# Performance work log

Hardware: AMD Instinct MI355X
Metric: run time of the kernel (lower is better)

The kernel has to match this reference:

```python
import jax, jax.numpy as jnp
import numpy as np

BN_EPS = 1e-5
ATT_EPS = 1e-6


def _conv(x, w, groups=1):
    # x: [B,C,H,W], w: [O, C//groups, k, k], stride 1, SAME padding for odd k
    k = w.shape[-1]
    p = (k - 1) // 2
    return jax.lax.conv_general_dilated(
        x, w, window_strides=(1, 1), padding=[(p, p), (p, p)],
        dimension_numbers=('NCHW', 'OIHW', 'NCHW'), feature_group_count=groups)


def _bn(x, bnp):
    # bnp: [4, C] stacked (scale, bias, running_mean, running_var); eval-mode BN
    s, b, m, v = bnp[0], bnp[1], bnp[2], bnp[3]
    inv = s / jnp.sqrt(v + BN_EPS)
    return x * inv[None, :, None, None] + (b - m * inv)[None, :, None, None]


def _relu6(x):
    return jnp.clip(x, 0.0, 6.0)


def _ffn(x, fc1_w, fc1_bn, conv1_w, conv1_bn, conv2_w, conv2_bn, fc2_w, fc2_bn):
    # E_FFN: 1x1 ConvBNReLU6 -> dw5x5 ConvBNReLU6 & dw3x3 ConvBNReLU6 -> sum -> 1x1 ConvBN -> ReLU6
    C = x.shape[1]
    h = _relu6(_bn(_conv(x, fc1_w), fc1_bn))
    x1 = _relu6(_bn(_conv(h, conv1_w, groups=C), conv1_bn))
    x2 = _relu6(_bn(_conv(h, conv2_w, groups=C), conv2_bn))
    return _relu6(_bn(_conv(x1 + x2, fc2_w), fc2_bn))


def _bias(y, b):
    return y + b[None, :, None, None]


def setup_inputs() -> dict:
    key = jax.random.key(0)
    ks = jax.random.split(key, 16)
    C, M = 64, 8  # in_places, in_places // scale
    B, H, W = 4, 224, 224

    def w(k, shape, s=0.05):
        return (jax.random.normal(k, shape, dtype=jnp.float32) * s)

    def bn_params(k, c):
        k1, k2, k3, k4 = jax.random.split(k, 4)
        scale = 1.0 + 0.1 * jax.random.normal(k1, (c,), dtype=jnp.float32)
        bias = 0.1 * jax.random.normal(k2, (c,), dtype=jnp.float32)
        mean = 0.1 * jax.random.normal(k3, (c,), dtype=jnp.float32)
        var = 1.0 + 0.1 * jax.random.uniform(k4, (c,), dtype=jnp.float32)
        return jnp.stack([scale, bias, mean, var])  # [4, c]

    return {
        'x': jax.random.normal(ks[0], (B, C, H, W), dtype=jnp.float32),
        'gamma': jnp.full((1,), 0.5, dtype=jnp.float32),  # nonzero so attention branch matters
        'q_w': w(ks[1], (M, C, 1, 1)), 'q_b': w(ks[2], (M,)),
        'k_w': w(ks[3], (M, C, 1, 1)), 'k_b': w(ks[4], (M,)),
        'v_w': w(ks[5], (C, C, 1, 1)), 'v_b': w(ks[6], (C,)),
        'fc1_w': w(ks[7], (C, C, 1, 1)), 'fc1_bn': bn_params(ks[8], C),
        'conv1_w': w(ks[9], (C, 1, 5, 5)), 'conv1_bn': bn_params(ks[10], C),
        'conv2_w': w(ks[11], (C, 1, 3, 3)), 'conv2_bn': bn_params(ks[12], C),
        'fc2_w': w(ks[13], (C, C, 1, 1)), 'fc2_bn': bn_params(ks[14], C),
    }


def reference(x, gamma, q_w, q_b, k_w, k_b, v_w, v_b,
              fc1_w, fc1_bn, conv1_w, conv1_bn, conv2_w, conv2_bn, fc2_w, fc2_bn):
    B, C, H, W = x.shape
    N = H * W
    x_channel = _ffn(x, fc1_w, fc1_bn, conv1_w, conv1_bn, conv2_w, conv2_bn, fc2_w, fc2_bn)
    # softplus feature maps; Q,K: [B, m, N]
    Q = jax.nn.softplus(_bias(_conv(x, q_w), q_b).reshape(B, -1, N))
    K = jax.nn.softplus(_bias(_conv(x, k_w), k_b).reshape(B, -1, N))
    V = (_bias(_conv(x, v_w), v_b) + x_channel).reshape(B, C, N)
    Qt = jnp.swapaxes(Q, 1, 2)                              # [B, N, m]
    KV = jnp.einsum('bmn,bcn->bmc', K, V)                   # [B, m, C]
    norm = 1.0 / jnp.einsum('bnm,bm->bn', Qt, K.sum(-1) + ATT_EPS)  # [B, N]
    wv = jnp.einsum('bnm,bmc,bn->bcn', Qt, KV, norm).reshape(B, C, H, W)
    return x + gamma * wv
```

## Files before the change

### kernel.cpp

```cpp
#include <hip/hip_runtime.h>
#include <math.h>

#define B_ 4
#define C_ 64
#define M_ 8
#define H_ 224
#define W_ 224
#define N_ (H_*W_)
#define CN_ (C_*N_)
#define MN_ (M_*N_)
#define BCN_ (B_*CN_)
#define BMN_ (B_*MN_)

typedef __attribute__((ext_vector_type(8))) short short8;
typedef __attribute__((ext_vector_type(4))) float f32x4;
typedef __attribute__((ext_vector_type(4))) unsigned int uint4v;

__device__ __forceinline__ float relu6f(float v){ return fminf(fmaxf(v,0.0f),6.0f); }
__device__ __forceinline__ float softplusf(float v){
  return v > 0.0f ? v + log1pf(expf(-v)) : log1pf(expf(v));
}
__device__ __forceinline__ unsigned int rne2(float lo, float hi){
  unsigned int ul = __float_as_uint(lo); ul += 0x7FFFu + ((ul>>16)&1u);
  unsigned int uh = __float_as_uint(hi); uh += 0x7FFFu + ((uh>>16)&1u);
  return (ul>>16) | (uh & 0xFFFF0000u);
}

#define FMA4(A, W, X) { A.x = fmaf((W), (X).x, A.x); A.y = fmaf((W), (X).y, A.y); \
                        A.z = fmaf((W), (X).z, A.z); A.w = fmaf((W), (X).w, A.w); }

__global__ __launch_bounds__(256) void k_fc1k(const float* __restrict__ x,
                                              const float* __restrict__ w,
                                              const float* __restrict__ bn,
                                              const float* __restrict__ kw,
                                              const float* __restrict__ kb,
                                              float* __restrict__ h,
                                              float* __restrict__ Kq)
{
  __shared__ float xsl[2*1024];
  __shared__ float wl [2*512];
  __shared__ float kt [512];
  const int tid  = threadIdx.x;
  const int b    = blockIdx.x / 392;
  const int pg   = blockIdx.x % 392;
  const int pix0 = pg*128;
  const float* xb = x + (size_t)b*CN_ + pix0;

  for (int idx = tid; idx < 512; idx += 256) {
    const int c = idx >> 3, m = idx & 7;
    kt[idx] = kw[m*64 + c];
  }

  const int scp = tid >> 5;
  const int spx = (tid & 31) << 2;
  const int e0 = tid*2, e1 = tid*2+1;
  const int wc0 = e0 >> 6, wo0 = e0 & 63;
  const int wc1 = e1 >> 6, wo1 = e1 & 63;

  {
    const float4 xr = *(const float4*)(xb + (size_t)scp*N_ + spx);
    const float w0r = w[wo0*64 + wc0];
    const float w1r = w[wo1*64 + wc1];
    *(float4*)&xsl[scp*128 + spx] = xr;
    wl[e0] = w0r; wl[e1] = w1r;
  }
  __syncthreads();

  const int lane = tid & 63, wv_ = tid >> 6;
  const int och  = 2*wv_ + (lane >> 5);
  const int ocb  = och*8;
  const int px4  = (lane & 31) << 2;

  float4 ah[8];
  float4 ak = {0,0,0,0};
  #pragma unroll
  for (int i = 0; i < 8; ++i) ah[i] = make_float4(0.f,0.f,0.f,0.f);

  for (int ck = 0; ck < 8; ++ck) {
    const int cur = ck & 1, nxt = cur ^ 1;
    const float* xc = &xsl[cur*1024];
    const float* wc = &wl[cur*512];
    float4 xr; float w0r, w1r;
    if (ck < 7) {
      const int c0n = (ck+1)*8;
      xr  = *(const float4*)(xb + (size_t)(c0n + scp)*N_ + spx);
      w0r = w[wo0*64 + c0n + wc0];
      w1r = w[wo1*64 + c0n + wc1];
    }
    #pragma unroll
    for (int cp = 0; cp < 8; ++cp) {
      const float4 xv = *(const float4*)&xc[cp*128 + px4];
      const float4 w0 = *(const float4*)&wc[cp*64 + ocb];
      const float4 w1 = *(const float4*)&wc[cp*64 + ocb + 4];
      const float kvw = kt[(ck*8+cp)*8 + och];
      FMA4(ah[0], w0.x, xv); FMA4(ah[1], w0.y, xv);
      FMA4(ah[2], w0.z, xv); FMA4(ah[3], w0.w, xv);
      FMA4(ah[4], w1.x, xv); FMA4(ah[5], w1.y, xv);
      FMA4(ah[6], w1.z, xv); FMA4(ah[7], w1.w, xv);
      FMA4(ak, kvw, xv);
    }
    if (ck < 7) {
      *(float4*)&xsl[nxt*1024 + scp*128 + spx] = xr;
      wl[nxt*512 + e0] = w0r; wl[nxt*512 + e1] = w1r;
    }
    __syncthreads();
  }

  float* hb = h + (size_t)b*CN_ + pix0 + px4;
  #pragma unroll
  for (int o = 0; o < 8; ++o) {
    const int oc = ocb + o;
    const float inv  = bn[oc] / sqrtf(bn[192+oc] + 1e-5f);
    const float beta = bn[64+oc] - bn[128+oc]*inv;
    float4 o4;
    o4.x = relu6f(fmaf(ah[o].x, inv, beta));
    o4.y = relu6f(fmaf(ah[o].y, inv, beta));
    o4.z = relu6f(fmaf(ah[o].z, inv, beta));
    o4.w = relu6f(fmaf(ah[o].w, inv, beta));
    *(float4*)(hb + (size_t)oc*N_) = o4;
  }
  {
    const float kbm = kb[och];
    float4 q;
    q.x = softplusf(ak.x + kbm); q.y = softplusf(ak.y + kbm);
    q.z = softplusf(ak.z + kbm); q.w = softplusf(ak.w + kbm);
    *(float4*)(Kq + (size_t)b*MN_ + (size_t)och*N_ + pix0 + px4) = q;
  }
}

__global__ __launch_bounds__(256) void k_dw(const float* __restrict__ h,
                                            const float* __restrict__ w5,
                                            const float* __restrict__ w3,
                                            const float* __restrict__ bn1,
                                            const float* __restrict__ bn2,
                                            float* __restrict__ s)
{
  __shared__ float tile[36*37];
  const int tid = threadIdx.x;
  const int blk = blockIdx.x;
  const int t   = blk % 49;
  const int bc  = blk / 49;
  const int c   = bc & 63;
  const int tx0 = (t % 7) * 32;
  const int ty0 = (t / 7) * 32;
  const float* hb = h + (size_t)bc * N_;

  for (int idx = tid; idx < 1296; idx += 256) {
    const int ly = idx / 36, lx = idx - ly*36;
    const int gy = ty0 + ly - 2, gx = tx0 + lx - 2;
    float v = 0.0f;
    if (gy >= 0 && gy < H_ && gx >= 0 && gx < W_) v = hb[gy*W_ + gx];
    tile[ly*37 + lx] = v;
  }
  __syncthreads();

  float w5r[25], w3r[9];
  #pragma unroll
  for (int i = 0; i < 25; ++i) w5r[i] = w5[c*25 + i];
  #pragma unroll
  for (int i = 0; i < 9; ++i)  w3r[i] = w3[c*9 + i];
  const float inv1 = bn1[c] / sqrtf(bn1[192+c] + 1e-5f);
  const float bet1 = bn1[64+c] - bn1[128+c]*inv1;
  const float inv2 = bn2[c] / sqrtf(bn2[192+c] + 1e-5f);
  const float bet2 = bn2[64+c] - bn2[128+c]*inv2;

  const int ty  = tid >> 3;
  const int tx4 = (tid & 7) << 2;
  float a5[4] = {0,0,0,0}, a3[4] = {0,0,0,0};
  #pragma unroll
  for (int dy = 0; dy < 5; ++dy) {
    float r[8];
    #pragma unroll
    for (int i = 0; i < 8; ++i) r[i] = tile[(ty+dy)*37 + tx4 + i];
    #pragma unroll
    for (int dx = 0; dx < 5; ++dx) {
      const float wv = w5r[dy*5+dx];
      #pragma unroll
      for (int p = 0; p < 4; ++p) a5[p] = fmaf(wv, r[p+dx], a5[p]);
    }
    if (dy >= 1 && dy <= 3) {
      #pragma unroll
      for (int dx = 1; dx <= 3; ++dx) {
        const float wv = w3r[(dy-1)*3+(dx-1)];
        #pragma unroll
        for (int p = 0; p < 4; ++p) a3[p] = fmaf(wv, r[p+dx], a3[p]);
      }
    }
  }
  float* sb = s + (size_t)bc * N_ + (ty0+ty)*W_ + tx0 + tx4;
  float4 o4;
  o4.x = relu6f(fmaf(a5[0],inv1,bet1)) + relu6f(fmaf(a3[0],inv2,bet2));
  o4.y = relu6f(fmaf(a5[1],inv1,bet1)) + relu6f(fmaf(a3[1],inv2,bet2));
  o4.z = relu6f(fmaf(a5[2],inv1,bet1)) + relu6f(fmaf(a3[2],inv2,bet2));
  o4.w = relu6f(fmaf(a5[3],inv1,bet1)) + relu6f(fmaf(a3[3],inv2,bet2));
  *(float4*)sb = o4;
}

__device__ __forceinline__ short8 bfrag(const unsigned short* __restrict__ L,
                                        int px, int c0){
  const unsigned short* p = L + c0*128 + px;
  unsigned int w0 = (unsigned int)p[0]   | ((unsigned int)p[128]<<16);
  unsigned int w1 = (unsigned int)p[256] | ((unsigned int)p[384]<<16);
  unsigned int w2 = (unsigned int)p[512] | ((unsigned int)p[640]<<16);
  unsigned int w3 = (unsigned int)p[768] | ((unsigned int)p[896]<<16);
  uint4v q = {w0,w1,w2,w3};
  return __builtin_bit_cast(short8, q);
}
__device__ __forceinline__ short8 afrag(const float* __restrict__ W, int idx){
  const float4 f0 = *(const float4*)(W + idx);
  const float4 f1 = *(const float4*)(W + idx + 4);
  uint4v q = {rne2(f0.x,f0.y), rne2(f0.z,f0.w), rne2(f1.x,f1.y), rne2(f1.z,f1.w)};
  return __builtin_bit_cast(short8, q);
}

__global__ __launch_bounds__(256) void k_v(const float* __restrict__ x,
                                           const float* __restrict__ s,
                                           const float* __restrict__ vw,
                                           const float* __restrict__ vb,
                                           const float* __restrict__ fw,
                                           const float* __restrict__ fbn,
                                           float* __restrict__ V)
{
  __shared__ unsigned short xls[64*128];
  __shared__ unsigned short sls[64*128];
  __shared__ float invb[3][64];
  const int tid  = threadIdx.x;
  const int b    = blockIdx.x / 392;
  const int pg   = blockIdx.x % 392;
  const int pix0 = pg*128;
  const float* xb = x + (size_t)b*CN_ + pix0;
  const float* sb = s + (size_t)b*CN_ + pix0;

  const int scp = tid >> 5;
  const int spx = (tid & 31) << 2;
  #pragma unroll
  for (int i = 0; i < 8; ++i) {
    const int c = i*8 + scp;
    const float4 xr = *(const float4*)(xb + (size_t)c*N_ + spx);
    const float4 sr = *(const float4*)(sb + (size_t)c*N_ + spx);
    *(uint2*)&xls[c*128 + spx] = make_uint2(rne2(xr.x,xr.y), rne2(xr.z,xr.w));
    *(uint2*)&sls[c*128 + spx] = make_uint2(rne2(sr.x,sr.y), rne2(sr.z,sr.w));
  }
  if (tid < 64) {
    const float inv = fbn[tid] / sqrtf(fbn[192+tid] + 1e-5f);
    invb[0][tid] = inv;
    invb[1][tid] = fbn[64+tid] - fbn[128+tid]*inv;
    invb[2][tid] = vb[tid];
  }
  __syncthreads();

  const int lane = tid & 63, wv = tid >> 6;
  const int l15 = lane & 15, u = lane >> 4;
  const int pxw = wv*32;

  f32x4 av[4][2], af[4][2];
  #pragma unroll
  for (int t = 0; t < 4; ++t)
    #pragma unroll
    for (int s2 = 0; s2 < 2; ++s2) { av[t][s2] = (f32x4){0.f,0.f,0.f,0.f};
                                     af[t][s2] = (f32x4){0.f,0.f,0.f,0.f}; }

  #pragma unroll
  for (int kk = 0; kk < 2; ++kk) {
    const int c0 = kk*32 + u*8;
    {
      const short8 a0 = afrag(vw, (0*16+l15)*64 + c0);
      const short8 a1 = afrag(vw, (1*16+l15)*64 + c0);
      const short8 a2 = afrag(vw, (2*16+l15)*64 + c0);
      const short8 a3 = afrag(vw, (3*16+l15)*64 + c0);
      #pragma unroll
      for (int s2 = 0; s2 < 2; ++s2) {
        const short8 bx = bfrag(xls, pxw + s2*16 + l15, c0);
        av[0][s2] = __builtin_amdgcn_mfma_f32_16x16x32_bf16(a0, bx, av[0][s2], 0,0,0);
        av[1][s2] = __builtin_amdgcn_mfma_f32_16x16x32_bf16(a1, bx, av[1][s2], 0,0,0);
        av[2][s2] = __builtin_amdgcn_mfma_f32_16x16x32_bf16(a2, bx, av[2][s2], 0,0,0);
        av[3][s2] = __builtin_amdgcn_mfma_f32_16x16x32_bf16(a3, bx, av[3][s2], 0,0,0);
      }
    }
    {
      const short8 a0 = afrag(fw, (0*16+l15)*64 + c0);
      const short8 a1 = afrag(fw, (1*16+l15)*64 + c0);
      const short8 a2 = afrag(fw, (2*16+l15)*64 + c0);
      const short8 a3 = afrag(fw, (3*16+l15)*64 + c0);
      #pragma unroll
      for (int s2 = 0; s2 < 2; ++s2) {
        const short8 bs = bfrag(sls, pxw + s2*16 + l15, c0);
        af[0][s2] = __builtin_amdgcn_mfma_f32_16x16x32_bf16(a0, bs, af[0][s2], 0,0,0);
        af[1][s2] = __builtin_amdgcn_mfma_f32_16x16x32_bf16(a1, bs, af[1][s2], 0,0,0);
        af[2][s2] = __builtin_amdgcn_mfma_f32_16x16x32_bf16(a2, bs, af[2][s2], 0,0,0);
        af[3][s2] = __builtin_amdgcn_mfma_f32_16x16x32_bf16(a3, bs, af[3][s2], 0,0,0);
      }
    }
  }

  float* Vb = V + (size_t)b*CN_ + pix0;
  #pragma unroll
  for (int t = 0; t < 4; ++t) {
    #pragma unroll
    for (int s2 = 0; s2 < 2; ++s2) {
      const int px = pxw + s2*16 + l15;
      #pragma unroll
      for (int r = 0; r < 4; ++r) {
        const int oc = t*16 + u*4 + r;
        Vb[(size_t)oc*N_ + px] = av[t][s2][r] + invb[2][oc]
            + relu6f(fmaf(af[t][s2][r], invb[0][oc], invb[1][oc]));
      }
    }
  }
}

__global__ __launch_bounds__(256) void k_kv(const float* __restrict__ V,
                                            const float* __restrict__ Kq,
                                            float* __restrict__ KV,
                                            float* __restrict__ Ksum)
{
  const int blk = blockIdx.x;
  const int b   = blk >> 7;
  const int rem = blk & 127;
  const int cg  = rem >> 4;
  const int ch  = rem & 15;
  const int tid = threadIdx.x;
  const int base = ch * 3136;
  const int end  = base + 3136;
  const float* Kb = Kq + (size_t)b*MN_;
  const float* Vb = V  + (size_t)b*CN_ + (size_t)(cg*8)*N_;

  float acc[64];
  #pragma unroll
  for (int i = 0; i < 64; ++i) acc[i] = 0.0f;
  float ks[8] = {0,0,0,0,0,0,0,0};

  for (int n4 = base + tid*4; n4 < end; n4 += 1024) {
    float4 kr[8];
    #pragma unroll
    for (int m2 = 0; m2 < 8; ++m2) kr[m2] = *(const float4*)(Kb + (size_t)m2*N_ + n4);
    #pragma unroll
    for (int m2 = 0; m2 < 8; ++m2)
      ks[m2] += (kr[m2].x + kr[m2].y) + (kr[m2].z + kr[m2].w);
    #pragma unroll
    for (int c8 = 0; c8 < 8; ++c8) {
      const float4 vv = *(const float4*)(Vb + (size_t)c8*N_ + n4);
      #pragma unroll
      for (int m2 = 0; m2 < 8; ++m2) {
        float t = acc[m2*8+c8];
        t = fmaf(kr[m2].x, vv.x, t);
        t = fmaf(kr[m2].y, vv.y, t);
        t = fmaf(kr[m2].z, vv.z, t);
        t = fmaf(kr[m2].w, vv.w, t);
        acc[m2*8+c8] = t;
      }
    }
  }
  const int lane = tid & 63;

  {
    int nv = 64;
    #pragma unroll
    for (int mask = 1; mask <= 32; mask <<= 1) {
      nv >>= 1;
      const bool hi = (lane & mask) != 0;
      #pragma unroll
      for (int i = 0; i < 32; ++i) {
        if (i < nv) {
          const float mine = hi ? acc[i] : acc[i+nv];
          const float th = __shfl_xor(mine, mask);
          acc[i] = (hi ? acc[i+nv] : acc[i]) + th;
        }
      }
    }
  }
  const int j = 32*(lane & 1) + 16*((lane >> 1) & 1) + 8*((lane >> 2) & 1)
              + 4*((lane >> 3) & 1) + 2*((lane >> 4) & 1) + ((lane >> 5) & 1);
  atomicAdd(&KV[b*512 + (j >> 3)*64 + cg*8 + (j & 7)], acc[0]);

  if (cg == 0) {
    float mk = 0.0f;
    #pragma unroll
    for (int jj = 0; jj < 8; ++jj) {
      float v = ks[jj];
      v += __shfl_xor(v, 1);
      v += __shfl_xor(v, 2);
      v += __shfl_xor(v, 4);
      v += __shfl_xor(v, 8);
      v += __shfl_xor(v, 16);
      v += __shfl_xor(v, 32);
      if (lane == jj) mk = v;
    }
    if (lane < 8) atomicAdd(&Ksum[b*8 + lane], mk);
  }
}

__global__ __launch_bounds__(256) void k_out(const float* __restrict__ x,
                                             const float* __restrict__ qw,
                                             const float* __restrict__ qb,
                                             const float* __restrict__ gamma,
                                             const float* __restrict__ KV,
                                             const float* __restrict__ Ksum,
                                             float* __restrict__ out)
{
  __shared__ float xs[64*128];
  __shared__ __align__(16) float kvt[64*8];
  __shared__ __align__(16) float qwt[64*8];
  __shared__ float qs[8][128];
  __shared__ float scl[128];
  __shared__ float ksl[8];
  const int tid = threadIdx.x;
  const int b  = blockIdx.x / 392;
  const int pg = blockIdx.x % 392;
  const int pix0 = pg*128;
  const float* xb = x + (size_t)b*CN_ + pix0;

  for (int idx = tid; idx < 512; idx += 256) {
    const int m = idx >> 6, c = idx & 63;
    kvt[c*8 + m] = KV[b*512 + idx];
    qwt[c*8 + m] = qw[idx];
  }
  if (tid < 8) ksl[tid] = Ksum[b*8 + tid] + 1e-6f;
  #pragma unroll
  for (int i = 0; i < 8; ++i) {
    const int idx = i*256 + tid;
    const int c = idx >> 5, p4 = (idx & 31) << 2;
    const float4 v = *(const float4*)(xb + (size_t)c*N_ + p4);
    *(float4*)&xs[c*128 + p4] = v;
  }
  __syncthreads();

  if (tid < 128) {
    const int px = tid;
    float q[8] = {0,0,0,0,0,0,0,0};
    #pragma unroll 8
    for (int c = 0; c < 64; ++c) {
      const float xv = xs[c*128 + px];
      const float4 w0 = *(const float4*)&qwt[c*8];
      const float4 w1 = *(const float4*)&qwt[c*8+4];
      q[0] = fmaf(w0.x, xv, q[0]);
      q[1] = fmaf(w0.y, xv, q[1]);
      q[2] = fmaf(w0.z, xv, q[2]);
      q[3] = fmaf(w0.w, xv, q[3]);
      q[4] = fmaf(w1.x, xv, q[4]);
      q[5] = fmaf(w1.y, xv, q[5]);
      q[6] = fmaf(w1.z, xv, q[6]);
      q[7] = fmaf(w1.w, xv, q[7]);
    }
    float den = 0.0f;
    #pragma unroll
    for (int m = 0; m < 8; ++m) {
      q[m] = softplusf(q[m] + qb[m]);
      den  = fmaf(q[m], ksl[m], den);
      qs[m][px] = q[m];
    }
    scl[px] = gamma[0] / den;
  }
  __syncthreads();

  float* ob = out + (size_t)b*CN_ + pix0;
  #pragma unroll
  for (int i = 0; i < 32; ++i) {
    const int idx = i*256 + tid;
    const int c = idx >> 7, px = idx & 127;
    const float4 k0 = *(const float4*)&kvt[c*8];
    const float4 k1 = *(const float4*)&kvt[c*8+4];
    float wv;
    wv = qs[0][px]*k0.x;
    wv = fmaf(qs[1][px], k0.y, wv);
    wv = fmaf(qs[2][px], k0.z, wv);
    wv = fmaf(qs[3][px], k0.w, wv);
    wv = fmaf(qs[4][px], k1.x, wv);
    wv = fmaf(qs[5][px], k1.y, wv);
    wv = fmaf(qs[6][px], k1.z, wv);
    wv = fmaf(qs[7][px], k1.w, wv);
    ob[(size_t)c*N_ + px] = fmaf(scl[px], wv, xs[c*128 + px]);
  }
}

extern "C" void kernel_launch(void* const* d_in, const int* in_sizes, int n_in,
                              void* d_out, int out_size, void* d_ws, size_t ws_size,
                              hipStream_t stream) {
  const float* x      = (const float*)d_in[0];
  const float* gamma  = (const float*)d_in[1];
  const float* q_w    = (const float*)d_in[2];
  const float* q_b    = (const float*)d_in[3];
  const float* k_w    = (const float*)d_in[4];
  const float* k_b    = (const float*)d_in[5];
  const float* v_w    = (const float*)d_in[6];
  const float* v_b    = (const float*)d_in[7];
  const float* fc1_w  = (const float*)d_in[8];
  const float* fc1_bn = (const float*)d_in[9];
  const float* c1_w   = (const float*)d_in[10];
  const float* c1_bn  = (const float*)d_in[11];
  const float* c2_w   = (const float*)d_in[12];
  const float* c2_bn  = (const float*)d_in[13];
  const float* fc2_w  = (const float*)d_in[14];
  const float* fc2_bn = (const float*)d_in[15];
  float* outp = (float*)d_out;

  float* ws   = (float*)d_ws;
  float* bufA = ws;
  float* bufS = ws + (size_t)BCN_;
  float* bufK = ws + (size_t)2*BCN_;
  float* kv   = ws + (size_t)2*BCN_ + BMN_;
  float* ksum = kv + 2048;

  hipMemsetAsync(kv, 0, (2048 + 32)*sizeof(float), stream);

  k_fc1k<<<dim3(B_*392), dim3(256), 0, stream>>>(x, fc1_w, fc1_bn, k_w, k_b, bufA, bufK);
  k_dw  <<<dim3(B_*C_*49), dim3(256), 0, stream>>>(bufA, c1_w, c2_w, c1_bn, c2_bn, bufS);
  k_v   <<<dim3(B_*392), dim3(256), 0, stream>>>(x, bufS, v_w, v_b, fc2_w, fc2_bn, bufA);
  k_kv  <<<dim3(512), dim3(256), 0, stream>>>(bufA, bufK, kv, ksum);
  k_out <<<dim3(B_*392), dim3(256), 0, stream>>>(x, q_w, q_b, gamma, kv, ksum, outp);
}
```

Measured before the change: 302.4 us.

## Compute fc1 and K projections with bf16 MFMA instead of fp32 FMAs

The fused fc1+K 1x1 conv kernel is rewritten to stage x as bf16 in shared memory and run the 64x64 fc1 and 8x64 K projections on 16x16x32 bf16 MFMA instructions, with the K rows padded into a fifth A tile. This replaces the fp32 FMA loop and its double-buffered x/weight staging. BN scale and shift are precomputed per block into shared memory. Output stores become scalar per-pixel writes rather than float4, and bf16 rounding of x and the weights reduces precision.

```diff
diff --git a/kernel.cpp b/kernel.cpp
--- a/kernel.cpp
+++ b/kernel.cpp
@@ -26,8 +26,26 @@
   return (ul>>16) | (uh & 0xFFFF0000u);
 }
 
-#define FMA4(A, W, X) { A.x = fmaf((W), (X).x, A.x); A.y = fmaf((W), (X).y, A.y); \
-                        A.z = fmaf((W), (X).z, A.z); A.w = fmaf((W), (X).w, A.w); }
+__device__ __forceinline__ short8 bfrag(const unsigned short* __restrict__ L,
+                                        int px, int c0){
+  const unsigned short* p = L + c0*128 + px;
+  unsigned int w0 = (unsigned int)p[0]   | ((unsigned int)p[128]<<16);
+  unsigned int w1 = (unsigned int)p[256] | ((unsigned int)p[384]<<16);
+  unsigned int w2 = (unsigned int)p[512] | ((unsigned int)p[640]<<16);
+  unsigned int w3 = (unsigned int)p[768] | ((unsigned int)p[896]<<16);
+  uint4v q = {w0,w1,w2,w3};
+  return __builtin_bit_cast(short8, q);
+}
+__device__ __forceinline__ short8 afrag(const float* __restrict__ W, int idx){
+  const float4 f0 = *(const float4*)(W + idx);
+  const float4 f1 = *(const float4*)(W + idx + 4);
+  uint4v q = {rne2(f0.x,f0.y), rne2(f0.z,f0.w), rne2(f1.x,f1.y), rne2(f1.z,f1.w)};
+  return __builtin_bit_cast(short8, q);
+}
+__device__ __forceinline__ short8 zfrag(){
+  uint4v q = {0u,0u,0u,0u};
+  return __builtin_bit_cast(short8, q);
+}
 
 __global__ __launch_bounds__(256) void k_fc1k(const float* __restrict__ x,
                                               const float* __restrict__ w,
@@ -37,94 +55,82 @@
                                               float* __restrict__ h,
                                               float* __restrict__ Kq)
 {
-  __shared__ float xsl[2*1024];
-  __shared__ float wl [2*512];
-  __shared__ float kt [512];
+  __shared__ unsigned short xls[64*128];
+  __shared__ float invb[2][64];
   const int tid  = threadIdx.x;
   const int b    = blockIdx.x / 392;
   const int pg   = blockIdx.x % 392;
   const int pix0 = pg*128;
   const float* xb = x + (size_t)b*CN_ + pix0;
 
-  for (int idx = tid; idx < 512; idx += 256) {
-    const int c = idx >> 3, m = idx & 7;
-    kt[idx] = kw[m*64 + c];
-  }
-
   const int scp = tid >> 5;
   const int spx = (tid & 31) << 2;
-  const int e0 = tid*2, e1 = tid*2+1;
-  const int wc0 = e0 >> 6, wo0 = e0 & 63;
-  const int wc1 = e1 >> 6, wo1 = e1 & 63;
-
-  {
-    const float4 xr = *(const float4*)(xb + (size_t)scp*N_ + spx);
-    const float w0r = w[wo0*64 + wc0];
-    const float w1r = w[wo1*64 + wc1];
-    *(float4*)&xsl[scp*128 + spx] = xr;
-    wl[e0] = w0r; wl[e1] = w1r;
+  #pragma unroll
+  for (int i = 0; i < 8; ++i) {
+    const int c = i*8 + scp;
+    const float4 xr = *(const float4*)(xb + (size_t)c*N_ + spx);
+    *(uint2*)&xls[c*128 + spx] = make_uint2(rne2(xr.x,xr.y), rne2(xr.z,xr.w));
+  }
+  if (tid < 64) {
+    const float inv = bn[tid] / sqrtf(bn[192+tid] + 1e-5f);
+    invb[0][tid] = inv;
+    invb[1][tid] = bn[64+tid] - bn[128+tid]*inv;
   }
   __syncthreads();
 
-  const int lane = tid & 63, wv_ = tid >> 6;
-  const int och  = 2*wv_ + (lane >> 5);
-  const int ocb  = och*8;
-  const int px4  = (lane & 31) << 2;
-
-  float4 ah[8];
-  float4 ak = {0,0,0,0};
-  #pragma unroll
-  for (int i = 0; i < 8; ++i) ah[i] = make_float4(0.f,0.f,0.f,0.f);
-
-  for (int ck = 0; ck < 8; ++ck) {
-    const int cur = ck & 1, nxt = cur ^ 1;
-    const float* xc = &xsl[cur*1024];
-    const float* wc = &wl[cur*512];
-    float4 xr; float w0r, w1r;
-    if (ck < 7) {
-      const int c0n = (ck+1)*8;
-      xr  = *(const float4*)(xb + (size_t)(c0n + scp)*N_ + spx);
-      w0r = w[wo0*64 + c0n + wc0];
-      w1r = w[wo1*64 + c0n + wc1];
-    }
-    #pragma unroll
-    for (int cp = 0; cp < 8; ++cp) {
-      const float4 xv = *(const float4*)&xc[cp*128 + px4];
-      const float4 w0 = *(const float4*)&wc[cp*64 + ocb];
-      const float4 w1 = *(const float4*)&wc[cp*64 + ocb + 4];
-      const float kvw = kt[(ck*8+cp)*8 + och];
-      FMA4(ah[0], w0.x, xv); FMA4(ah[1], w0.y, xv);
-      FMA4(ah[2], w0.z, xv); FMA4(ah[3], w0.w, xv);
-      FMA4(ah[4], w1.x, xv); FMA4(ah[5], w1.y, xv);
-      FMA4(ah[6], w1.z, xv); FMA4(ah[7], w1.w, xv);
-      FMA4(ak, kvw, xv);
-    }
-    if (ck < 7) {
-      *(float4*)&xsl[nxt*1024 + scp*128 + spx] = xr;
-      wl[nxt*512 + e0] = w0r; wl[nxt*512 + e1] = w1r;
-    }
-    __syncthreads();
-  }
-
-  float* hb = h + (size_t)b*CN_ + pix0 + px4;
-  #pragma unroll
-  for (int o = 0; o < 8; ++o) {
-    const int oc = ocb + o;
-    const float inv  = bn[oc] / sqrtf(bn[192+oc] + 1e-5f);
-    const float beta = bn[64+oc] - bn[128+oc]*inv;
-    float4 o4;
-    o4.x = relu6f(fmaf(ah[o].x, inv, beta));
-    o4.y = relu6f(fmaf(ah[o].y, inv, beta));
-    o4.z = relu6f(fmaf(ah[o].z, inv, beta));
-    o4.w = relu6f(fmaf(ah[o].w, inv, beta));
-    *(float4*)(hb + (size_t)oc*N_) = o4;
-  }
-  {
-    const float kbm = kb[och];
-    float4 q;
-    q.x = softplusf(ak.x + kbm); q.y = softplusf(ak.y + kbm);
-    q.z = softplusf(ak.z + kbm); q.w = softplusf(ak.w + kbm);
-    *(float4*)(Kq + (size_t)b*MN_ + (size_t)och*N_ + pix0 + px4) = q;
+  const int lane = tid & 63, wv = tid >> 6;
+  const int l15 = lane & 15, u = lane >> 4;
+  const int pxw = wv*32;
+
+  f32x4 acc[5][2];
+  #pragma unroll
+  for (int t = 0; t < 5; ++t)
+    #pragma unroll
+    for (int s2 = 0; s2 < 2; ++s2) acc[t][s2] = (f32x4){0.f,0.f,0.f,0.f};
+
+  #pragma unroll
+  for (int kk = 0; kk < 2; ++kk) {
+    const int c0 = kk*32 + u*8;
+    const short8 a0 = afrag(w, (0*16+l15)*64 + c0);
+    const short8 a1 = afrag(w, (1*16+l15)*64 + c0);
+    const short8 a2 = afrag(w, (2*16+l15)*64 + c0);
+    const short8 a3 = afrag(w, (3*16+l15)*64 + c0);
+    const short8 a4 = (l15 < 8) ? afrag(kw, l15*64 + c0) : zfrag();
+    #pragma unroll
+    for (int s2 = 0; s2 < 2; ++s2) {
+      const short8 bx = bfrag(xls, pxw + s2*16 + l15, c0);
+      acc[0][s2] = __builtin_amdgcn_mfma_f32_16x16x32_bf16(a0, bx, acc[0][s2], 0,0,0);
+      acc[1][s2] = __builtin_amdgcn_mfma_f32_16x16x32_bf16(a1, bx, acc[1][s2], 0,0,0);
+      acc[2][s2] = __builtin_amdgcn_mfma_f32_16x16x32_bf16(a2, bx, acc[2][s2], 0,0,0);
+      acc[3][s2] = __builtin_amdgcn_mfma_f32_16x16x32_bf16(a3, bx, acc[3][s2], 0,0,0);
+      acc[4][s2] = __builtin_amdgcn_mfma_f32_16x16x32_bf16(a4, bx, acc[4][s2], 0,0,0);
+    }
+  }
+
+  float* hb = h + (size_t)b*CN_ + pix0;
+  #pragma unroll
+  for (int t = 0; t < 4; ++t) {
+    #pragma unroll
+    for (int s2 = 0; s2 < 2; ++s2) {
+      const int px = pxw + s2*16 + l15;
+      #pragma unroll
+      for (int r = 0; r < 4; ++r) {
+        const int oc = t*16 + u*4 + r;
+        hb[(size_t)oc*N_ + px] = relu6f(fmaf(acc[t][s2][r], invb[0][oc], invb[1][oc]));
+      }
+    }
+  }
+  if (u < 2) {
+    float* Kb = Kq + (size_t)b*MN_ + pix0;
+    #pragma unroll
+    for (int s2 = 0; s2 < 2; ++s2) {
+      const int px = pxw + s2*16 + l15;
+      #pragma unroll
+      for (int r = 0; r < 4; ++r) {
+        const int m = u*4 + r;
+        Kb[(size_t)m*N_ + px] = softplusf(acc[4][s2][r] + kb[m]);
+      }
+    }
   }
 }
 
@@ -194,23 +200,6 @@
   o4.z = relu6f(fmaf(a5[2],inv1,bet1)) + relu6f(fmaf(a3[2],inv2,bet2));
   o4.w = relu6f(fmaf(a5[3],inv1,bet1)) + relu6f(fmaf(a3[3],inv2,bet2));
   *(float4*)sb = o4;
-}
-
-__device__ __forceinline__ short8 bfrag(const unsigned short* __restrict__ L,
-                                        int px, int c0){
-  const unsigned short* p = L + c0*128 + px;
-  unsigned int w0 = (unsigned int)p[0]   | ((unsigned int)p[128]<<16);
-  unsigned int w1 = (unsigned int)p[256] | ((unsigned int)p[384]<<16);
-  unsigned int w2 = (unsigned int)p[512] | ((unsigned int)p[640]<<16);
-  unsigned int w3 = (unsigned int)p[768] | ((unsigned int)p[896]<<16);
-  uint4v q = {w0,w1,w2,w3};
-  return __builtin_bit_cast(short8, q);
-}
-__device__ __forceinline__ short8 afrag(const float* __restrict__ W, int idx){
-  const float4 f0 = *(const float4*)(W + idx);
-  const float4 f1 = *(const float4*)(W + idx + 4);
-  uint4v q = {rne2(f0.x,f0.y), rne2(f0.z,f0.w), rne2(f1.x,f1.y), rne2(f1.z,f1.w)};
-  return __builtin_bit_cast(short8, q);
 }
 
 __global__ __launch_bounds__(256) void k_v(const float* __restrict__ x,
```

Result: no change. 301.5 us (-0.3%).
